# Optimization experiments

Measured on AMD Instinct MI355X. Metric: run time of the kernel, lower is better.

Reference implementation:

```python
import jax, jax.numpy as jnp
import numpy as np

PATCH_LENGTH = 128
PATCH_STRIDE = 64
WINDOW_SIZE = 16
L = 500000


def setup_inputs() -> dict:
    key = jax.random.key(0)
    k1, k2, k3 = jax.random.split(key, 3)
    I = jax.random.normal(k1, (L,), dtype=jnp.float32)
    Q = jax.random.normal(k2, (L,), dtype=jnp.float32)
    edge_weights = jax.random.normal(k3, (PATCH_LENGTH, PATCH_LENGTH), dtype=jnp.float32)
    return {"I": I, "Q": Q, "edge_weights": edge_weights}


def reference(I, Q, edge_weights):
    pl, stride, ws = PATCH_LENGTH, PATCH_STRIDE, WINDOW_SIZE
    n = I.shape[0]
    P = (n - pl) // stride + 1
    # Gather all patches at once: idx[p, t] = p*stride + t  -> [P, pl]
    idx = jnp.arange(P)[:, None] * stride + jnp.arange(pl)[None, :]
    patches = jnp.stack([I[idx], Q[idx]], axis=-1)  # [P, pl, 2]
    # Banded adjacency computed ONCE (it is identical for every patch):
    # adj[i, j] = sigmoid(edge_weights[i, j]) if 0 < |i - j| <= ws else 0
    r = jnp.arange(pl)
    d = jnp.abs(r[:, None] - r[None, :])
    band_mask = ((d <= ws) & (d > 0)).astype(edge_weights.dtype)  # [pl, pl]
    adj = jax.nn.sigmoid(edge_weights) * band_mask
    adjs = jnp.broadcast_to(adj, (P, pl, pl))  # [P, pl, pl]
    return patches, adjs
```

## Files before the change

kernel.cpp:

```cpp
#include <hip/hip_runtime.h>

#define PL 128
#define STRIDE 64
#define WSZ 16

typedef float f32x4 __attribute__((ext_vector_type(4)));

__global__ __launch_bounds__(256) void fused_kernel(
    const float* __restrict__ I, const float* __restrict__ Q,
    const float* __restrict__ ew, float* __restrict__ out, int P)
{
    const int tid  = threadIdx.x;
    const int bid  = blockIdx.x;
    const int nblk = gridDim.x;

    {
        f32x4* pout = reinterpret_cast<f32x4*>(out);
        const int total = P * (PL / 2);
        for (int idx = bid * 256 + tid; idx < total; idx += nblk * 256) {
            int p = idx >> 6;
            int t = (idx & 63) * 2;
            int src = p * STRIDE + t;
            f32x4 val = {I[src], Q[src], I[src + 1], Q[src + 1]};
            __builtin_nontemporal_store(val, &pout[idx]);
        }
    }

    f32x4 v[16];
#pragma unroll
    for (int k = 0; k < 16; ++k) {
        const int i  = k * 8 + (tid >> 5);
        const int j0 = (tid & 31) * 4;
        f32x4 r = {0.f, 0.f, 0.f, 0.f};
#pragma unroll
        for (int c = 0; c < 4; ++c) {
            int j = j0 + c;
            int d = i - j; if (d < 0) d = -d;
            if (d > 0 && d <= WSZ) {
                r[c] = 1.0f / (1.0f + __expf(-ew[i * PL + j]));
            }
        }
        v[k] = r;
    }

    f32x4* aout = reinterpret_cast<f32x4*>(out + (size_t)P * PL * 2);
    int p0 = bid * 4;
    int p1 = p0 + 4; if (p1 > P) p1 = P;
    for (int p = p0; p < p1; ++p) {
        f32x4* dst = aout + (size_t)p * (PL * PL / 4);
#pragma unroll
        for (int k = 0; k < 16; ++k) {
            __builtin_nontemporal_store(v[k], &dst[k * 256 + tid]);
        }
    }
}

extern "C" void kernel_launch(void* const* d_in, const int* in_sizes, int n_in,
                              void* d_out, int out_size, void* d_ws, size_t ws_size,
                              hipStream_t stream) {
    const float* I  = (const float*)d_in[0];
    const float* Q  = (const float*)d_in[1];
    const float* ew = (const float*)d_in[2];
    float* out = (float*)d_out;

    const int n = in_sizes[0];
    const int P = (n - PL) / STRIDE + 1;

    const int nblk = (P + 3) / 4;
    fused_kernel<<<nblk, 256, 0, stream>>>(I, Q, ew, out, P);
}
```

Baseline: 107.3 us.

## Use fixed grid with grid-stride adjacency broadcast and per-block row rotation

Replaces the one-block-per-four-patches launch with a fixed grid of 1009 blocks that write the broadcast adjacency tensor in a flat grid-stride pattern. Each block precomputes its 16 row vectors, rotated by block index, so that consecutive stride steps land on the right row because the grid size is congruent to 1 mod 16. The goal is to cut block launch overhead and spread the streaming stores more evenly across memory channels. It relies on that modular property of the grid size and adds a bounds-checked tail loop.

```diff
diff --git a/kernel.cpp b/kernel.cpp
--- a/kernel.cpp
+++ b/kernel.cpp
@@ -10,47 +10,59 @@
     const float* __restrict__ I, const float* __restrict__ Q,
     const float* __restrict__ ew, float* __restrict__ out, int P)
 {
-    const int tid  = threadIdx.x;
-    const int bid  = blockIdx.x;
-    const int nblk = gridDim.x;
+    const int tid = threadIdx.x;
+    const int bid = blockIdx.x;
+    const unsigned T = gridDim.x * 256;
+    const unsigned idx0 = bid * 256 + tid;
 
     {
         f32x4* pout = reinterpret_cast<f32x4*>(out);
-        const int total = P * (PL / 2);
-        for (int idx = bid * 256 + tid; idx < total; idx += nblk * 256) {
-            int p = idx >> 6;
-            int t = (idx & 63) * 2;
+        const unsigned total = (unsigned)P * (PL / 2);
+        for (unsigned idx = idx0; idx < total; idx += T) {
+            int p = (int)(idx >> 6);
+            int t = ((int)idx & 63) * 2;
             int src = p * STRIDE + t;
             f32x4 val = {I[src], Q[src], I[src + 1], Q[src + 1]};
             __builtin_nontemporal_store(val, &pout[idx]);
         }
     }
 
+    const int r = bid & 15;
     f32x4 v[16];
 #pragma unroll
-    for (int k = 0; k < 16; ++k) {
-        const int i  = k * 8 + (tid >> 5);
-        const int j0 = (tid & 31) * 4;
-        f32x4 r = {0.f, 0.f, 0.f, 0.f};
+    for (int i = 0; i < 16; ++i) {
+        const int kk  = (r + i) & 15;
+        const int row = kk * 8 + (tid >> 5);
+        const int j0  = (tid & 31) * 4;
+        f32x4 val = {0.f, 0.f, 0.f, 0.f};
 #pragma unroll
         for (int c = 0; c < 4; ++c) {
             int j = j0 + c;
-            int d = i - j; if (d < 0) d = -d;
+            int d = row - j; if (d < 0) d = -d;
             if (d > 0 && d <= WSZ) {
-                r[c] = 1.0f / (1.0f + __expf(-ew[i * PL + j]));
+                val[c] = 1.0f / (1.0f + __expf(-ew[row * PL + j]));
             }
         }
-        v[k] = r;
+        v[i] = val;
     }
 
     f32x4* aout = reinterpret_cast<f32x4*>(out + (size_t)P * PL * 2);
-    int p0 = bid * 4;
-    int p1 = p0 + 4; if (p1 > P) p1 = P;
-    for (int p = p0; p < p1; ++p) {
-        f32x4* dst = aout + (size_t)p * (PL * PL / 4);
+    const unsigned M = (unsigned)P * (PL * PL / 4);
+    unsigned m = idx0;
+
+    const long long lim = (long long)M - 15LL * T;
+    while ((long long)m < lim) {
 #pragma unroll
-        for (int k = 0; k < 16; ++k) {
-            __builtin_nontemporal_store(v[k], &dst[k * 256 + tid]);
+        for (int i = 0; i < 16; ++i) {
+            __builtin_nontemporal_store(v[i], &aout[m]);
+            m += T;
+        }
+    }
+    while (m < M) {
+#pragma unroll
+        for (int i = 0; i < 16; ++i) {
+            if (m < M) __builtin_nontemporal_store(v[i], &aout[m]);
+            m += T;
         }
     }
 }
@@ -66,6 +78,6 @@
     const int n = in_sizes[0];
     const int P = (n - PL) / STRIDE + 1;
 
-    const int nblk = (P + 3) / 4;
-    fused_kernel<<<nblk, 256, 0, stream>>>(I, Q, ew, out, P);
+    const int gridB = 1009;
+    fused_kernel<<<gridB, 256, 0, stream>>>(I, Q, ew, out, P);
 }
```

Result: slower. 112.5 us (+4.9%).
